# Kernel optimization log

Hardware: AMD Instinct MI355X
Metric: run time of the kernel (lower is better)

Reference implementation:

```python
import jax, jax.numpy as jnp
import numpy as np

B, S, D, H = 2, 2048, 1024, 16
HD = D // H  # head_dim = 64


def setup_inputs() -> dict:
    key = jax.random.key(0)
    ks = jax.random.split(key, 6)
    scale_h = 1.0 / np.sqrt(HD)
    scale_d = 1.0 / np.sqrt(D)
    return {
        "x": jax.random.normal(ks[0], (B, S, D), dtype=jnp.float32),
        # per-head projection weights (CausalAttention Linear(head_dim, head_dim, bias=False)), stacked over heads
        "Wq": jax.random.normal(ks[1], (H, HD, HD), dtype=jnp.float32) * scale_h,
        "Wk": jax.random.normal(ks[2], (H, HD, HD), dtype=jnp.float32) * scale_h,
        "Wv": jax.random.normal(ks[3], (H, HD, HD), dtype=jnp.float32) * scale_h,
        # final nn.Linear(dim, dim): y = x @ Wo + bo (Wo stored already transposed vs torch)
        "Wo": jax.random.normal(ks[4], (D, D), dtype=jnp.float32) * scale_d,
        "bo": jax.random.normal(ks[5], (D,), dtype=jnp.float32) * 0.01,
    }


def reference(x, Wq, Wk, Wv, Wo, bo):
    b, s, d = x.shape
    h, hd, _ = Wq.shape
    # head h sees contiguous channel slice x[:, :, h*hd:(h+1)*hd]
    xh = x.reshape(b, s, h, hd)                                  # [B,S,H,HD]
    q = jnp.einsum("bshd,hde->bhse", xh, Wq)                     # [B,H,S,HD]
    k = jnp.einsum("bshd,hde->bhse", xh, Wk)
    v = jnp.einsum("bshd,hde->bhse", xh, Wv)
    scores = jnp.einsum("bhse,bhte->bhst", q, k) * (hd ** -0.5)  # [B,H,S,S]
    causal = jnp.tril(jnp.ones((s, s), dtype=bool))
    scores = jnp.where(causal, scores, jnp.finfo(scores.dtype).min)
    attn = jax.nn.softmax(scores, axis=-1)
    out = jnp.einsum("bhst,bhtd->bshd", attn, v)                 # [B,S,H,HD]
    # torch.stack(out_list, dim=-1) -> [B,S,HD,H]; reshape -> interleaved channels
    out = jnp.swapaxes(out, -1, -2).reshape(b, s, d)
    return out @ Wo + bo
```

## Files before the change

kernel.cpp:

```cpp
#include <hip/hip_runtime.h>

typedef __attribute__((ext_vector_type(8))) _Float16 half8;
typedef __attribute__((ext_vector_type(2))) __fp16 fp16x2;
typedef __attribute__((ext_vector_type(4))) float f32x4;
typedef __attribute__((ext_vector_type(16))) float f32x16;

constexpr int Bc = 2, Sc = 2048, Dc = 1024, Hc = 16, HDc = 64;

__device__ __forceinline__ int swz(int row, int colh) {
  return row * 64 + (colh ^ ((row & 7) * 8));
}

#define PKU(a, b) __builtin_bit_cast(unsigned, __builtin_amdgcn_cvt_pkrtz((a), (b)))

#define PACK_STORE(vA0, vA1, vA2, vA3, vB0, vB1, vB2, vB3, ptr) {        \
  unsigned W0 = PKU(vA0, vA1), W1 = PKU(vA2, vA3);                       \
  unsigned X0 = PKU(vB0, vB1), X1 = PKU(vB2, vB3);                       \
  unsigned s0_ = (unsigned)__shfl_xor((int)(hi ? W0 : X0), 32);          \
  unsigned s1_ = (unsigned)__shfl_xor((int)(hi ? W1 : X1), 32);          \
  union { unsigned u[4]; half8 h8; } P_;                                 \
  P_.u[0] = hi ? s0_ : W0; P_.u[1] = hi ? s1_ : W1;                      \
  P_.u[2] = hi ? X0 : s0_; P_.u[3] = hi ? X1 : s1_;                      \
  *(half8*)(ptr) = P_.h8; }

__global__ __launch_bounds__(256) void prep_w(const float* __restrict__ Wq,
                                              const float* __restrict__ Wk,
                                              const float* __restrict__ Wv,
                                              _Float16* __restrict__ WT) {
  const int m = blockIdx.x >> 4;
  const int h = blockIdx.x & 15;
  const float* src = (m == 0 ? Wq : (m == 1 ? Wk : Wv)) + (size_t)h * 4096;
  const float scale = (m == 0) ? 0.125f * 1.44269504088896f : 1.0f;
  __shared__ float T[64][65];
  const int tid = threadIdx.x;
#pragma unroll
  for (int i = 0; i < 4; ++i) {
    int r = (tid >> 4) + 16 * i, c4 = (tid & 15) * 4;
    *(float4*)&T[r][c4] = *(const float4*)(src + r * 64 + c4);
  }
  __syncthreads();
  _Float16* dst = WT + ((size_t)m * 16 + h) * 4096;
#pragma unroll
  for (int i = 0; i < 4; ++i) {
    int e = (tid >> 4) + 16 * i, d4 = (tid & 15) * 4;
    union { _Float16 hh[4]; unsigned long long u; } pk;
#pragma unroll
    for (int j = 0; j < 4; ++j) pk.hh[j] = (_Float16)(T[d4 + j][e] * scale);
    *(unsigned long long*)(dst + (size_t)e * 64 + d4) = pk.u;
  }
}

__global__ __launch_bounds__(256) void prep_wo(const float* __restrict__ Wo,
                                               _Float16* __restrict__ WoT) {
  __shared__ float T[64][68];
  const int hh = blockIdx.x;
  const int n0 = blockIdx.y * 64;
  const int tid = threadIdx.x;
#pragma unroll
  for (int i = 0; i < 4; ++i) {
    int g = tid + i * 256;
    int e = g >> 4, c4 = (g & 15) * 4;
    *(float4*)&T[e][c4] = *(const float4*)(Wo + (size_t)(e * 16 + hh) * Dc + n0 + c4);
  }
  __syncthreads();
#pragma unroll
  for (int i = 0; i < 4; ++i) {
    int g = tid + i * 256;
    int c = g >> 4, e4 = (g & 15) * 4;
    union { _Float16 h[4]; unsigned long long u; } pk;
    pk.h[0] = (_Float16)T[e4 + 0][c];
    pk.h[1] = (_Float16)T[e4 + 1][c];
    pk.h[2] = (_Float16)T[e4 + 2][c];
    pk.h[3] = (_Float16)T[e4 + 3][c];
    *(unsigned long long*)(WoT + (size_t)(n0 + c) * Dc + hh * 64 + e4) = pk.u;
  }
}

__global__ __launch_bounds__(256) void qkv_proj(
    const float* __restrict__ x, const _Float16* __restrict__ WT,
    _Float16* __restrict__ Qp, _Float16* __restrict__ Kp,
    _Float16* __restrict__ Vp) {
  const int h = blockIdx.x & 15;
  const int st = (blockIdx.x >> 4) & 15;
  const int b = blockIdx.x >> 8;
  const int s0 = st * 128;
  __shared__ __align__(16) _Float16 xs[128 * 64];
  const int tid = threadIdx.x;
#pragma unroll
  for (int i = 0; i < 4; ++i) {
    int r = (tid >> 3) + 32 * i;
    int c8 = (tid & 7) * 8;
    const float* xp = x + ((size_t)(b * Sc + s0 + r)) * Dc + h * 64 + c8;
    float4 u0 = *(const float4*)xp;
    float4 u1 = *(const float4*)(xp + 4);
    union { fp16x2 h2[4]; half8 h8; } pk;
    pk.h2[0] = __builtin_amdgcn_cvt_pkrtz(u0.x, u0.y);
    pk.h2[1] = __builtin_amdgcn_cvt_pkrtz(u0.z, u0.w);
    pk.h2[2] = __builtin_amdgcn_cvt_pkrtz(u1.x, u1.y);
    pk.h2[3] = __builtin_amdgcn_cvt_pkrtz(u1.z, u1.w);
    *(half8*)&xs[swz(r, c8)] = pk.h8;
  }
  __syncthreads();
  const int l = tid & 63, w = tid >> 6;
  const int lq = l & 31, hi = l >> 5;
  half8 xa[4];
#pragma unroll
  for (int c = 0; c < 4; ++c)
    xa[c] = *(const half8*)&xs[swz(32 * w + lq, c * 16 + hi * 8)];

  const _Float16* WTq = WT + (size_t)h * 4096;
  const _Float16* WTk = WT + (size_t)(16 + h) * 4096;
  const _Float16* WTv = WT + (size_t)(32 + h) * 4096;
  f32x16 Qt[2] = {}, Kt[2] = {}, Vd[2] = {};
#pragma unroll
  for (int et = 0; et < 2; ++et) {
#pragma unroll
    for (int c = 0; c < 4; ++c) {
      const int off = (32 * et + lq) * 64 + c * 16 + hi * 8;
      half8 wqf = *(const half8*)(WTq + off);
      half8 wkf = *(const half8*)(WTk + off);
      half8 wvf = *(const half8*)(WTv + off);
      Qt[et] = __builtin_amdgcn_mfma_f32_32x32x16_f16(wqf, xa[c], Qt[et], 0, 0, 0);
      Kt[et] = __builtin_amdgcn_mfma_f32_32x32x16_f16(wkf, xa[c], Kt[et], 0, 0, 0);
      Vd[et] = __builtin_amdgcn_mfma_f32_32x32x16_f16(xa[c], wvf, Vd[et], 0, 0, 0);
    }
  }
  const int bh = b * Hc + h;
  const int qt_ = 4 * st + w;
  const int ktile = 2 * st + (w >> 1);
  _Float16* qdst = Qp + (((size_t)(bh * 64 + qt_) * 4) << 9) + (l << 3);
  _Float16* kdst = Kp + (((size_t)((bh * 32 + ktile) * 8) + (w & 1) * 4) << 9) + (l << 3);
  _Float16* vdst = Vp + (((size_t)(bh * 32 + ktile) * 8) << 9) + (l << 3);

  PACK_STORE(Qt[0][0], Qt[0][1], Qt[0][2], Qt[0][3], Qt[0][4], Qt[0][5], Qt[0][6], Qt[0][7], qdst + (0 << 9));
  PACK_STORE(Qt[0][8], Qt[0][9], Qt[0][10], Qt[0][11], Qt[0][12], Qt[0][13], Qt[0][14], Qt[0][15], qdst + (1 << 9));
  PACK_STORE(Qt[1][0], Qt[1][1], Qt[1][2], Qt[1][3], Qt[1][4], Qt[1][5], Qt[1][6], Qt[1][7], qdst + (2 << 9));
  PACK_STORE(Qt[1][8], Qt[1][9], Qt[1][10], Qt[1][11], Qt[1][12], Qt[1][13], Qt[1][14], Qt[1][15], qdst + (3 << 9));

  PACK_STORE(Kt[0][0], Kt[0][1], Kt[0][2], Kt[0][3], Kt[0][4], Kt[0][5], Kt[0][6], Kt[0][7], kdst + (0 << 9));
  PACK_STORE(Kt[0][8], Kt[0][9], Kt[0][10], Kt[0][11], Kt[0][12], Kt[0][13], Kt[0][14], Kt[0][15], kdst + (1 << 9));
  PACK_STORE(Kt[1][0], Kt[1][1], Kt[1][2], Kt[1][3], Kt[1][4], Kt[1][5], Kt[1][6], Kt[1][7], kdst + (2 << 9));
  PACK_STORE(Kt[1][8], Kt[1][9], Kt[1][10], Kt[1][11], Kt[1][12], Kt[1][13], Kt[1][14], Kt[1][15], kdst + (3 << 9));

#pragma unroll
  for (int et = 0; et < 2; ++et) {
    PACK_STORE(Vd[et][0], Vd[et][1], Vd[et][2], Vd[et][3], Vd[et][4], Vd[et][5], Vd[et][6], Vd[et][7],
               vdst + ((size_t)(et * 4 + ((2 * w + 0) & 3)) << 9));
    PACK_STORE(Vd[et][8], Vd[et][9], Vd[et][10], Vd[et][11], Vd[et][12], Vd[et][13], Vd[et][14], Vd[et][15],
               vdst + ((size_t)(et * 4 + ((2 * w + 1) & 3)) << 9));
  }
}

#define DOB(t, q0v) (((t) * 64 + 32) <= (q0v) + 31)

#define LOADK(KA, KB, t, q0v) {                                               \
  const _Float16* p8 = Kp + (((kvb + (t)) * 8) << 9) + (l << 3);              \
  _Pragma("unroll") for (int c = 0; c < 4; ++c)                               \
    KA[c] = *(const half8*)(p8 + (c << 9));                                   \
  if (DOB(t, q0v)) {                                                          \
    _Pragma("unroll") for (int c = 0; c < 4; ++c)                             \
      KB[c] = *(const half8*)(p8 + ((4 + c) << 9));                           \
  } }

#define STEP(KA, KB, t, q0v) {                                                \
  const int k0 = (t) * 64;                                                    \
  const bool doB = DOB(t, q0v);                                               \
  const int q_g = (q0v) + lq;                                                 \
  const _Float16* vp8 = Vp + (((kvb + (t)) * 8) << 9) + (l << 3);             \
  half8 va[4], vb[4];                                                         \
  _Pragma("unroll") for (int c = 0; c < 4; ++c) {                             \
    va[c] = *(const half8*)(vp8 + (c << 9));                                  \
    vb[c] = *(const half8*)(vp8 + ((4 + c) << 9));                            \
  }                                                                           \
  f32x16 SA = {}, SB = {};                                                    \
  __builtin_amdgcn_s_setprio(1);                                              \
  _Pragma("unroll") for (int c = 0; c < 4; ++c)                               \
    SA = __builtin_amdgcn_mfma_f32_32x32x16_f16(KA[c], qf[c], SA, 0, 0, 0);   \
  if (doB) {                                                                  \
    _Pragma("unroll") for (int c = 0; c < 4; ++c)                             \
      SB = __builtin_amdgcn_mfma_f32_32x32x16_f16(KB[c], qf[c], SB, 0, 0, 0); \
  }                                                                           \
  __builtin_amdgcn_s_setprio(0);                                              \
  if (k0 + 63 > (q0v)) {                                                      \
    _Pragma("unroll") for (int r = 0; r < 16; ++r) {                          \
      const int kk = k0 + (r & 3) + 8 * (r >> 2) + 4 * hi;                    \
      if (kk > q_g) SA[r] = -1e30f;                                           \
      if (doB && kk + 32 > q_g) SB[r] = -1e30f;                               \
    }                                                                         \
  }                                                                           \
  float mx = -1e30f;                                                          \
  _Pragma("unroll") for (int r = 0; r < 16; ++r) mx = fmaxf(mx, SA[r]);       \
  if (doB) {                                                                  \
    _Pragma("unroll") for (int r = 0; r < 16; ++r) mx = fmaxf(mx, SB[r]);     \
  }                                                                           \
  mx = fmaxf(mx, __shfl_xor(mx, 32));                                         \
  if (!__all(mx <= m_run + 4.0f)) {                                           \
    const float mnew = fmaxf(m_run, mx);                                      \
    const float corr = __builtin_amdgcn_exp2f(m_run - mnew);                  \
    l_run *= corr;                                                            \
    _Pragma("unroll") for (int r = 0; r < 16; ++r) { OA[r] *= corr; OB[r] *= corr; } \
    m_run = mnew;                                                             \
  }                                                                           \
  float Pv[32];                                                               \
  float ls = 0.f;                                                             \
  _Pragma("unroll") for (int r = 0; r < 16; ++r) {                            \
    Pv[r] = __builtin_amdgcn_exp2f(SA[r] - m_run);                            \
    ls += Pv[r];                                                              \
  }                                                                           \
  if (doB) {                                                                  \
    _Pragma("unroll") for (int r = 0; r < 16; ++r) {                          \
      Pv[16 + r] = __builtin_amdgcn_exp2f(SB[r] - m_run);                     \
      ls += Pv[16 + r];                                                       \
    }                                                                         \
  }                                                                           \
  ls += __shfl_xor(ls, 32);                                                   \
  l_run += ls;                                                                \
  __builtin_amdgcn_s_setprio(1);                                              \
  _Pragma("unroll") for (int ch = 0; ch < 4; ++ch) {                          \
    if (ch < (doB ? 4 : 2)) {                                                 \
      unsigned W0 = PKU(Pv[ch * 8 + 0], Pv[ch * 8 + 1]);                      \
      unsigned W1 = PKU(Pv[ch * 8 + 2], Pv[ch * 8 + 3]);                      \
      unsigned W2 = PKU(Pv[ch * 8 + 4], Pv[ch * 8 + 5]);                      \
      unsigned W3 = PKU(Pv[ch * 8 + 6], Pv[ch * 8 + 7]);                      \
      unsigned sw0 = (unsigned)__shfl_xor((int)(hi ? W0 : W2), 32);           \
      unsigned sw1 = (unsigned)__shfl_xor((int)(hi ? W1 : W3), 32);           \
      union { unsigned u[4]; half8 h; } pa;                                   \
      pa.u[0] = hi ? sw0 : W0;                                                \
      pa.u[1] = hi ? sw1 : W1;                                                \
      pa.u[2] = hi ? W2 : sw0;                                                \
      pa.u[3] = hi ? W3 : sw1;                                                \
      OA = __builtin_amdgcn_mfma_f32_32x32x16_f16(va[ch], pa.h, OA, 0, 0, 0); \
      OB = __builtin_amdgcn_mfma_f32_32x32x16_f16(vb[ch], pa.h, OB, 0, 0, 0); \
    }                                                                         \
  }                                                                           \
  __builtin_amdgcn_s_setprio(0); }

#define RUN_RANGE(t0, t1, q0v) {                                              \
  int t = (t0);                                                               \
  LOADK(kaE, kbE, t, q0v);                                                    \
  for (; t + 2 <= (t1); t += 2) {                                             \
    LOADK(kaO, kbO, t + 1, q0v);                                              \
    STEP(kaE, kbE, t, q0v);                                                   \
    if (t + 2 < (t1)) { LOADK(kaE, kbE, t + 2, q0v); }                        \
    STEP(kaO, kbO, t + 1, q0v);                                               \
  }                                                                           \
  if (t < (t1)) { STEP(kaE, kbE, t, q0v); } }

__global__ __launch_bounds__(128, 2) void flash_attn(
    const _Float16* __restrict__ Qp, const _Float16* __restrict__ Kp,
    const _Float16* __restrict__ Vp, _Float16* __restrict__ attC) {
  const int i = blockIdx.x;
  const int bh = (i & 7) * 4 + ((i >> 3) & 3);
  const int p = i >> 5;
  const int qlong = 63 - p, qshort = p;
  const int NTL = qlong / 2 + 1;
  const int b = bh >> 4, h = bh & 15;
  const int tid = threadIdx.x;
  const int wv = tid >> 6, l = tid & 63;
  const int lq = l & 31, hi = l >> 5;
  const size_t kvb = (size_t)bh * 32;

  __shared__ __align__(16) float Osh[8][64][4];
  __shared__ float mlsh[2][64];

  half8 qf[4], kaE[4], kbE[4], kaO[4], kbO[4];
  f32x16 OA = {}, OB = {};
  float m_run = -1e30f, l_run = 0.f;

  if (wv == 0) {
    const int q0 = qlong * 32;
    const _Float16* qb = Qp + (((size_t)(bh * 64 + qlong) * 4) << 9) + (l << 3);
#pragma unroll
    for (int c = 0; c < 4; ++c) qf[c] = *(const half8*)(qb + (c << 9));
    RUN_RANGE(0, 16, q0);
  } else {
    const int q0s = qshort * 32;
    const int NTS = qshort / 2 + 1;
    const _Float16* qb = Qp + (((size_t)(bh * 64 + qshort) * 4) << 9) + (l << 3);
#pragma unroll
    for (int c = 0; c < 4; ++c) qf[c] = *(const half8*)(qb + (c << 9));
    RUN_RANGE(0, NTS, q0s);
    {
      const float inv = 1.f / l_run;
      _Float16* op = attC + ((size_t)b * Sc + q0s + lq) * Dc + h * 64;
#pragma unroll
      for (int g = 0; g < 4; ++g) {
        union { _Float16 hh[4]; unsigned long long u; } pA, pB;
#pragma unroll
        for (int jj = 0; jj < 4; ++jj) {
          pA.hh[jj] = (_Float16)(OA[4 * g + jj] * inv);
          pB.hh[jj] = (_Float16)(OB[4 * g + jj] * inv);
        }
        *(unsigned long long*)(op + 8 * g + 4 * hi) = pA.u;
        *(unsigned long long*)(op + 32 + 8 * g + 4 * hi) = pB.u;
      }
    }
    const int q0 = qlong * 32;
    const _Float16* qb2 = Qp + (((size_t)(bh * 64 + qlong) * 4) << 9) + (l << 3);
#pragma unroll
    for (int c = 0; c < 4; ++c) qf[c] = *(const half8*)(qb2 + (c << 9));
#pragma unroll
    for (int r = 0; r < 16; ++r) { OA[r] = 0.f; OB[r] = 0.f; }
    m_run = -1e30f; l_run = 0.f;
    RUN_RANGE(16, NTL, q0);
#pragma unroll
    for (int g = 0; g < 4; ++g) {
      float4 a, bq;
      a.x = OA[4 * g + 0]; a.y = OA[4 * g + 1]; a.z = OA[4 * g + 2]; a.w = OA[4 * g + 3];
      bq.x = OB[4 * g + 0]; bq.y = OB[4 * g + 1]; bq.z = OB[4 * g + 2]; bq.w = OB[4 * g + 3];
      *(float4*)&Osh[g][l][0] = a;
      *(float4*)&Osh[4 + g][l][0] = bq;
    }
    mlsh[0][l] = m_run;
    mlsh[1][l] = l_run;
  }
  __syncthreads();
  if (wv == 0) {
    const float m1 = mlsh[0][l], l1 = mlsh[1][l];
    const float mm = fmaxf(m_run, m1);
    const float c0 = __builtin_amdgcn_exp2f(m_run - mm);
    const float c1 = __builtin_amdgcn_exp2f(m1 - mm);
    const float linv = 1.f / (l_run * c0 + l1 * c1);
    _Float16* op = attC + ((size_t)b * Sc + qlong * 32 + lq) * Dc + h * 64;
#pragma unroll
    for (int g = 0; g < 4; ++g) {
      const float4 o1a = *(const float4*)&Osh[g][l][0];
      const float4 o1b = *(const float4*)&Osh[4 + g][l][0];
      union { _Float16 hh[4]; unsigned long long u; } pA, pB;
      pA.hh[0] = (_Float16)((OA[4 * g + 0] * c0 + o1a.x * c1) * linv);
      pA.hh[1] = (_Float16)((OA[4 * g + 1] * c0 + o1a.y * c1) * linv);
      pA.hh[2] = (_Float16)((OA[4 * g + 2] * c0 + o1a.z * c1) * linv);
      pA.hh[3] = (_Float16)((OA[4 * g + 3] * c0 + o1a.w * c1) * linv);
      pB.hh[0] = (_Float16)((OB[4 * g + 0] * c0 + o1b.x * c1) * linv);
      pB.hh[1] = (_Float16)((OB[4 * g + 1] * c0 + o1b.y * c1) * linv);
      pB.hh[2] = (_Float16)((OB[4 * g + 2] * c0 + o1b.z * c1) * linv);
      pB.hh[3] = (_Float16)((OB[4 * g + 3] * c0 + o1b.w * c1) * linv);
      *(unsigned long long*)(op + 8 * g + 4 * hi) = pA.u;
      *(unsigned long long*)(op + 32 + 8 * g + 4 * hi) = pB.u;
    }
  }
}

__global__ __launch_bounds__(256) void out_proj(
    const _Float16* __restrict__ attC, const _Float16* __restrict__ WoT,
    const float* __restrict__ bo, float* __restrict__ out) {
  const int m0 = blockIdx.x * 64, n0 = blockIdx.y * 128;
  __shared__ __align__(16) _Float16 Alds[64][40];
  __shared__ __align__(16) _Float16 Blds[128][40];
  const int tid = threadIdx.x;
  const int l = tid & 63, w = tid >> 6;
  const int lr = l & 15, lg = l >> 4;
  f32x4 acc[4][2] = {};
  for (int kt = 0; kt < 32; ++kt) {
    const int k0 = kt * 32;
    {
      const int r = tid >> 2, c8 = (tid & 3) * 8;
      *(half8*)&Alds[r][c8] = *(const half8*)(attC + (size_t)(m0 + r) * Dc + k0 + c8);
#pragma unroll
      for (int ii = 0; ii < 2; ++ii) {
        const int g = tid + ii * 256;
        const int rb = g >> 2, cb = (g & 3) * 8;
        *(half8*)&Blds[rb][cb] = *(const half8*)(WoT + (size_t)(n0 + rb) * Dc + k0 + cb);
      }
    }
    __syncthreads();
    half8 af[4], bf[2];
#pragma unroll
    for (int i2 = 0; i2 < 4; ++i2) af[i2] = *(const half8*)&Alds[i2 * 16 + lr][lg * 8];
#pragma unroll
    for (int j = 0; j < 2; ++j) bf[j] = *(const half8*)&Blds[w * 32 + j * 16 + lr][lg * 8];
#pragma unroll
    for (int i2 = 0; i2 < 4; ++i2)
#pragma unroll
      for (int j = 0; j < 2; ++j)
        acc[i2][j] = __builtin_amdgcn_mfma_f32_16x16x32_f16(af[i2], bf[j], acc[i2][j], 0, 0, 0);
    __syncthreads();
  }
#pragma unroll
  for (int i2 = 0; i2 < 4; ++i2)
#pragma unroll
    for (int j = 0; j < 2; ++j) {
      const int n = n0 + w * 32 + j * 16 + lr;
      const float bias = bo[n];
#pragma unroll
      for (int r = 0; r < 4; ++r) {
        const int m = m0 + i2 * 16 + lg * 4 + r;
        out[(size_t)m * Dc + n] = acc[i2][j][r] + bias;
      }
    }
}

extern "C" void kernel_launch(void* const* d_in, const int* in_sizes, int n_in,
                              void* d_out, int out_size, void* d_ws, size_t ws_size,
                              hipStream_t stream) {
  const float* x  = (const float*)d_in[0];
  const float* Wq = (const float*)d_in[1];
  const float* Wk = (const float*)d_in[2];
  const float* Wv = (const float*)d_in[3];
  const float* Wo = (const float*)d_in[4];
  const float* bo = (const float*)d_in[5];
  float* out = (float*)d_out;
  char* ws = (char*)d_ws;
  _Float16* Qp   = (_Float16*)(ws);
  _Float16* Kp   = (_Float16*)(ws + (size_t)(8  << 20));
  _Float16* Vp   = (_Float16*)(ws + (size_t)(16 << 20));
  _Float16* WoT  = (_Float16*)(ws + (size_t)(24 << 20));
  _Float16* WT   = (_Float16*)(ws + (size_t)(26 << 20));
  _Float16* attC = (_Float16*)(ws + (size_t)(26 << 20));

  prep_w<<<dim3(48), dim3(256), 0, stream>>>(Wq, Wk, Wv, WT);
  prep_wo<<<dim3(16, 16), dim3(256), 0, stream>>>(Wo, WoT);
  qkv_proj<<<dim3(512), dim3(256), 0, stream>>>(x, WT, Qp, Kp, Vp);
  flash_attn<<<dim3(1024), dim3(128), 0, stream>>>(Qp, Kp, Vp, attC);
  out_proj<<<dim3(64, 8), dim3(256), 0, stream>>>(attC, WoT, bo, out);
}
```

Before: 79.29 us.

## Split paired causal q-tiles across four waves with split-KV merge

```diff
diff --git a/kernel.cpp b/kernel.cpp
--- a/kernel.cpp
+++ b/kernel.cpp
@@ -152,6 +152,11 @@
 }
 
 #define DOB(t, q0v) (((t) * 64 + 32) <= (q0v) + 31)
+
+#define LOADQ(qtv) {                                                          \
+  const _Float16* qb_ = Qp + (((size_t)(bh * 64 + (qtv)) * 4) << 9) + (l << 3); \
+  _Pragma("unroll") for (int c = 0; c < 4; ++c)                               \
+    qf[c] = *(const half8*)(qb_ + (c << 9)); }
 
 #define LOADK(KA, KB, t, q0v) {                                               \
   const _Float16* p8 = Kp + (((kvb + (t)) * 8) << 9) + (l << 3);              \
@@ -246,7 +251,41 @@
   }                                                                           \
   if (t < (t1)) { STEP(kaE, kbE, t, q0v); } }
 
-__global__ __launch_bounds__(128, 2) void flash_attn(
+#define PUBLISH(slot) {                                                       \
+  _Pragma("unroll") for (int r = 0; r < 16; ++r) {                            \
+    Osh[slot][l][r] = OA[r]; Osh[slot][l][16 + r] = OB[r];                    \
+  }                                                                           \
+  mls[slot][0][l] = m_run; mls[slot][1][l] = l_run; }
+
+#define RESET() {                                                             \
+  _Pragma("unroll") for (int r = 0; r < 16; ++r) { OA[r] = 0.f; OB[r] = 0.f; } \
+  m_run = -1e30f; l_run = 0.f; }
+
+#define MERGE(slot) {                                                         \
+  const float ms = mls[slot][0][l], lsv = mls[slot][1][l];                    \
+  const float mm = fmaxf(m_run, ms);                                          \
+  const float c0 = __builtin_amdgcn_exp2f(m_run - mm);                        \
+  const float c1 = __builtin_amdgcn_exp2f(ms - mm);                           \
+  _Pragma("unroll") for (int r = 0; r < 16; ++r) {                            \
+    OA[r] = OA[r] * c0 + Osh[slot][l][r] * c1;                                \
+    OB[r] = OB[r] * c0 + Osh[slot][l][16 + r] * c1;                           \
+  }                                                                           \
+  l_run = l_run * c0 + lsv * c1; m_run = mm; }
+
+#define STORE_OUT(q0v) {                                                      \
+  const float inv = 1.f / l_run;                                              \
+  _Float16* op = attC + ((size_t)b * Sc + (q0v) + lq) * Dc + h * 64;          \
+  _Pragma("unroll") for (int g = 0; g < 4; ++g) {                             \
+    union { _Float16 hh[4]; unsigned long long u; } pA, pB;                   \
+    _Pragma("unroll") for (int jj = 0; jj < 4; ++jj) {                        \
+      pA.hh[jj] = (_Float16)(OA[4 * g + jj] * inv);                           \
+      pB.hh[jj] = (_Float16)(OB[4 * g + jj] * inv);                           \
+    }                                                                         \
+    *(unsigned long long*)(op + 8 * g + 4 * hi) = pA.u;                       \
+    *(unsigned long long*)(op + 32 + 8 * g + 4 * hi) = pB.u;                  \
+  } }
+
+__global__ __launch_bounds__(256, 4) void flash_attn(
     const _Float16* __restrict__ Qp, const _Float16* __restrict__ Kp,
     const _Float16* __restrict__ Vp, _Float16* __restrict__ attC) {
   const int i = blockIdx.x;
@@ -254,90 +293,62 @@
   const int p = i >> 5;
   const int qlong = 63 - p, qshort = p;
   const int NTL = qlong / 2 + 1;
+  const int NTS = qshort / 2 + 1;
+  const int q0L = qlong * 32, q0S = qshort * 32;
   const int b = bh >> 4, h = bh & 15;
   const int tid = threadIdx.x;
   const int wv = tid >> 6, l = tid & 63;
   const int lq = l & 31, hi = l >> 5;
   const size_t kvb = (size_t)bh * 32;
 
-  __shared__ __align__(16) float Osh[8][64][4];
-  __shared__ float mlsh[2][64];
+  __shared__ float Osh[3][64][33];
+  __shared__ float mls[3][2][64];
 
   half8 qf[4], kaE[4], kbE[4], kaO[4], kbO[4];
   f32x16 OA = {}, OB = {};
   float m_run = -1e30f, l_run = 0.f;
 
   if (wv == 0) {
-    const int q0 = qlong * 32;
-    const _Float16* qb = Qp + (((size_t)(bh * 64 + qlong) * 4) << 9) + (l << 3);
-#pragma unroll
-    for (int c = 0; c < 4; ++c) qf[c] = *(const half8*)(qb + (c << 9));
-    RUN_RANGE(0, 16, q0);
+    LOADQ(qlong);
+    RUN_RANGE(0, 8, q0L);
+  } else if (wv == 1) {
+    LOADQ(qlong);
+    RUN_RANGE(8, 16, q0L);
+    PUBLISH(0);
+  } else if (wv == 2) {
+    LOADQ(qlong);
+    const int e2 = NTL < 24 ? NTL : 24;
+    RUN_RANGE(16, e2, q0L);
+    PUBLISH(1);
+    RESET();
+    if (24 - NTL > 0) {
+      LOADQ(qshort);
+      RUN_RANGE(0, 24 - NTL, q0S);
+    }
   } else {
-    const int q0s = qshort * 32;
-    const int NTS = qshort / 2 + 1;
-    const _Float16* qb = Qp + (((size_t)(bh * 64 + qshort) * 4) << 9) + (l << 3);
-#pragma unroll
-    for (int c = 0; c < 4; ++c) qf[c] = *(const half8*)(qb + (c << 9));
-    RUN_RANGE(0, NTS, q0s);
-    {
-      const float inv = 1.f / l_run;
-      _Float16* op = attC + ((size_t)b * Sc + q0s + lq) * Dc + h * 64;
-#pragma unroll
-      for (int g = 0; g < 4; ++g) {
-        union { _Float16 hh[4]; unsigned long long u; } pA, pB;
-#pragma unroll
-        for (int jj = 0; jj < 4; ++jj) {
-          pA.hh[jj] = (_Float16)(OA[4 * g + jj] * inv);
-          pB.hh[jj] = (_Float16)(OB[4 * g + jj] * inv);
-        }
-        *(unsigned long long*)(op + 8 * g + 4 * hi) = pA.u;
-        *(unsigned long long*)(op + 32 + 8 * g + 4 * hi) = pB.u;
-      }
+    if (NTL > 24) {
+      LOADQ(qlong);
+      RUN_RANGE(24, NTL, q0L);
+      PUBLISH(2);
+      RESET();
+      LOADQ(qshort);
+      RUN_RANGE(0, NTS, q0S);
+      STORE_OUT(q0S);
+    } else {
+      LOADQ(qshort);
+      RUN_RANGE(24 - NTL, NTS, q0S);
+      PUBLISH(2);
     }
-    const int q0 = qlong * 32;
-    const _Float16* qb2 = Qp + (((size_t)(bh * 64 + qlong) * 4) << 9) + (l << 3);
-#pragma unroll
-    for (int c = 0; c < 4; ++c) qf[c] = *(const half8*)(qb2 + (c << 9));
-#pragma unroll
-    for (int r = 0; r < 16; ++r) { OA[r] = 0.f; OB[r] = 0.f; }
-    m_run = -1e30f; l_run = 0.f;
-    RUN_RANGE(16, NTL, q0);
-#pragma unroll
-    for (int g = 0; g < 4; ++g) {
-      float4 a, bq;
-      a.x = OA[4 * g + 0]; a.y = OA[4 * g + 1]; a.z = OA[4 * g + 2]; a.w = OA[4 * g + 3];
-      bq.x = OB[4 * g + 0]; bq.y = OB[4 * g + 1]; bq.z = OB[4 * g + 2]; bq.w = OB[4 * g + 3];
-      *(float4*)&Osh[g][l][0] = a;
-      *(float4*)&Osh[4 + g][l][0] = bq;
-    }
-    mlsh[0][l] = m_run;
-    mlsh[1][l] = l_run;
   }
   __syncthreads();
   if (wv == 0) {
-    const float m1 = mlsh[0][l], l1 = mlsh[1][l];
-    const float mm = fmaxf(m_run, m1);
-    const float c0 = __builtin_amdgcn_exp2f(m_run - mm);
-    const float c1 = __builtin_amdgcn_exp2f(m1 - mm);
-    const float linv = 1.f / (l_run * c0 + l1 * c1);
-    _Float16* op = attC + ((size_t)b * Sc + qlong * 32 + lq) * Dc + h * 64;
-#pragma unroll
-    for (int g = 0; g < 4; ++g) {
-      const float4 o1a = *(const float4*)&Osh[g][l][0];
-      const float4 o1b = *(const float4*)&Osh[4 + g][l][0];
-      union { _Float16 hh[4]; unsigned long long u; } pA, pB;
-      pA.hh[0] = (_Float16)((OA[4 * g + 0] * c0 + o1a.x * c1) * linv);
-      pA.hh[1] = (_Float16)((OA[4 * g + 1] * c0 + o1a.y * c1) * linv);
-      pA.hh[2] = (_Float16)((OA[4 * g + 2] * c0 + o1a.z * c1) * linv);
-      pA.hh[3] = (_Float16)((OA[4 * g + 3] * c0 + o1a.w * c1) * linv);
-      pB.hh[0] = (_Float16)((OB[4 * g + 0] * c0 + o1b.x * c1) * linv);
-      pB.hh[1] = (_Float16)((OB[4 * g + 1] * c0 + o1b.y * c1) * linv);
-      pB.hh[2] = (_Float16)((OB[4 * g + 2] * c0 + o1b.z * c1) * linv);
-      pB.hh[3] = (_Float16)((OB[4 * g + 3] * c0 + o1b.w * c1) * linv);
-      *(unsigned long long*)(op + 8 * g + 4 * hi) = pA.u;
-      *(unsigned long long*)(op + 32 + 8 * g + 4 * hi) = pB.u;
-    }
+    MERGE(0);
+    MERGE(1);
+    if (NTL > 24) { MERGE(2); }
+    STORE_OUT(q0L);
+  } else if (wv == 2 && NTL <= 24) {
+    MERGE(2);
+    STORE_OUT(q0S);
   }
 }
 
@@ -411,6 +422,6 @@
   prep_w<<<dim3(48), dim3(256), 0, stream>>>(Wq, Wk, Wv, WT);
   prep_wo<<<dim3(16, 16), dim3(256), 0, stream>>>(Wo, WoT);
   qkv_proj<<<dim3(512), dim3(256), 0, stream>>>(x, WT, Qp, Kp, Vp);
-  flash_attn<<<dim3(1024), dim3(128), 0, stream>>>(Qp, Kp, Vp, attC);
+  flash_attn<<<dim3(1024), dim3(256), 0, stream>>>(Qp, Kp, Vp, attC);
   out_proj<<<dim3(64, 8), dim3(256), 0, stream>>>(attC, WoT, bo, out);
 }
```

After: 210.8 us. +165.9%, slower.
